# Performance work log

Measured on AMD Instinct MI355X. Metric: run time of the kernel, lower is better.

The kernel has to match this reference:

```python
import jax, jax.numpy as jnp
import numpy as np

D_MODEL = 1024
H = 16
D_K = D_MODEL // H
NEG_INF = -1e9


def setup_inputs() -> dict:
    key = jax.random.key(0)
    ks = jax.random.split(key, 12)
    B, S = 2, 2048
    s = 1.0 / np.sqrt(D_MODEL)
    inp = {
        "query": jax.random.normal(ks[0], (B, S, D_MODEL), jnp.float32),
        "key": jax.random.normal(ks[1], (B, S, D_MODEL), jnp.float32),
        "value": jax.random.normal(ks[2], (B, S, D_MODEL), jnp.float32),
        "mask": jnp.ones((B, 1, 1, S), jnp.int32),
        "w_q": jax.random.normal(ks[3], (D_MODEL, D_MODEL), jnp.float32) * s,
        "b_q": jax.random.normal(ks[4], (D_MODEL,), jnp.float32) * s,
        "w_k": jax.random.normal(ks[5], (D_MODEL, D_MODEL), jnp.float32) * s,
        "b_k": jax.random.normal(ks[6], (D_MODEL,), jnp.float32) * s,
        "w_v": jax.random.normal(ks[7], (D_MODEL, D_MODEL), jnp.float32) * s,
        "b_v": jax.random.normal(ks[8], (D_MODEL,), jnp.float32) * s,
        "w_o": jax.random.normal(ks[9], (D_MODEL, D_MODEL), jnp.float32) * s,
        "b_o": jax.random.normal(ks[10], (D_MODEL,), jnp.float32) * s,
    }
    return inp


def _split_heads(x):
    B, S, _ = x.shape
    return x.reshape(B, S, H, D_K).transpose(0, 2, 1, 3)  # (B,H,S,d_k)


def reference(query, key, value, mask, w_q, b_q, w_k, b_k, w_v, b_v, w_o, b_o):
    # torch Linear: y = x @ W^T + b
    q = _split_heads(query @ w_q.T + b_q)
    k = _split_heads(key @ w_k.T + b_k)
    v = _split_heads(value @ w_v.T + b_v)
    scale = 1.0 / jnp.sqrt(jnp.asarray(D_K, q.dtype))
    scores = jnp.einsum("bhqd,bhkd->bhqk", q, k) * scale  # (B,H,Sq,Sk)
    scores = jnp.where(mask == 0, jnp.asarray(NEG_INF, scores.dtype), scores)
    attn = jax.nn.softmax(scores, axis=-1)
    ctx = jnp.einsum("bhqk,bhkd->bhqd", attn, v)
    B, _, Sq, _ = ctx.shape
    ctx = ctx.transpose(0, 2, 1, 3).reshape(B, Sq, D_MODEL)
    out = ctx @ w_o.T + b_o
    return out, attn
```

## Files before the change

kernel.cpp:

```cpp
#include <hip/hip_runtime.h>
#include <math.h>

#define MDIM 4096
#define NDIM 1024
#define KDIM 1024
#define S_LEN 2048
#define NH 16
#define DK 64
#define KT 64
#define QT 64
#define NTILE (S_LEN / KT)

__global__ __launch_bounds__(256)
void gemm_nt_kernel(const float* __restrict__ A, const float* __restrict__ W,
                    const float* __restrict__ bias, float* __restrict__ Y,
                    int split_head)
{
    __shared__ float As[16][68];
    __shared__ float Ws[16][68];
    const int tid = threadIdx.x;
    const int m0 = blockIdx.y << 6;
    const int n0 = blockIdx.x << 6;
    const int tx = tid & 15;
    const int ty = tid >> 4;

    float acc[4][4] = {};

    for (int k0 = 0; k0 < KDIM; k0 += 16) {
        #pragma unroll
        for (int i = 0; i < 4; i++) {
            int e = tid + (i << 8);
            int r = e >> 4;
            int c = e & 15;
            As[c][r] = A[(m0 + r) * KDIM + k0 + c];
            Ws[c][r] = W[(n0 + r) * KDIM + k0 + c];
        }
        __syncthreads();
        #pragma unroll
        for (int kk = 0; kk < 16; kk++) {
            float a[4], w[4];
            #pragma unroll
            for (int i = 0; i < 4; i++) a[i] = As[kk][ty * 4 + i];
            #pragma unroll
            for (int j = 0; j < 4; j++) w[j] = Ws[kk][tx * 4 + j];
            #pragma unroll
            for (int i = 0; i < 4; i++)
                #pragma unroll
                for (int j = 0; j < 4; j++)
                    acc[i][j] += a[i] * w[j];
        }
        __syncthreads();
    }

    #pragma unroll
    for (int i = 0; i < 4; i++) {
        int m = m0 + ty * 4 + i;
        #pragma unroll
        for (int j = 0; j < 4; j++) {
            int n = n0 + tx * 4 + j;
            float val = acc[i][j] + bias[n];
            if (split_head) {
                int b = m >> 11, s = m & (S_LEN - 1);
                int h = n >> 6,  d = n & (DK - 1);
                Y[(((size_t)(b * NH + h) * S_LEN + s) << 6) + d] = val;
            } else {
                Y[(size_t)m * NDIM + n] = val;
            }
        }
    }
}

__global__ __launch_bounds__(256, 3)
void attn_kernel(const float* __restrict__ q, const float* __restrict__ k,
                 const float* __restrict__ v, const int* __restrict__ mask,
                 float* __restrict__ attn, float* __restrict__ ctx)
{
    const int b   = blockIdx.z;
    const int h   = blockIdx.y;
    const int q0  = blockIdx.x << 6;
    const int tid = threadIdx.x;
    const int tx  = tid & 15;
    const int ty  = tid >> 4;

    __shared__ float Qs[64][68];
    __shared__ float Ks[64][68];
    __shared__ float Vs[64][68];
    float* Ps = &Ks[0][0];

    const float* qbase = q + (((size_t)(b * NH + h) * S_LEN + q0) << 6);
    const float* kbase = k + (((size_t)(b * NH + h) * S_LEN) << 6);
    const float* vbase = v + (((size_t)(b * NH + h) * S_LEN) << 6);
    const int*   mrow  = mask + b * S_LEN;

    const int ln = tid & 63;
    const int dg = tid >> 6;

    {
        const float4* src = (const float4*)(qbase + ((size_t)ln << 6) + (dg << 4));
        #pragma unroll
        for (int c4 = 0; c4 < 4; c4++) {
            float4 t = src[c4];
            int d = (dg << 4) + (c4 << 2);
            Qs[d + 0][ln] = t.x; Qs[d + 1][ln] = t.y;
            Qs[d + 2][ln] = t.z; Qs[d + 3][ln] = t.w;
        }
    }

    const float scale = 0.125f;
    float mr[4], lr[4];
    #pragma unroll
    for (int i = 0; i < 4; i++) { mr[i] = -1e30f; lr[i] = 0.f; }

    for (int t = 0; t < NTILE; t++) {
        float4 kr[4];
        {
            const float4* src = (const float4*)(kbase + (((size_t)(t << 6) + ln) << 6) + (dg << 4));
            #pragma unroll
            for (int c4 = 0; c4 < 4; c4++) kr[c4] = src[c4];
        }
        __syncthreads();
        #pragma unroll
        for (int c4 = 0; c4 < 4; c4++) {
            int d = (dg << 4) + (c4 << 2);
            Ks[d + 0][ln] = kr[c4].x; Ks[d + 1][ln] = kr[c4].y;
            Ks[d + 2][ln] = kr[c4].z; Ks[d + 3][ln] = kr[c4].w;
        }
        __syncthreads();

        float s[4][4] = {};
        #pragma unroll 8
        for (int kk = 0; kk < 64; kk++) {
            float a[4], w[4];
            *(float4*)a = *(const float4*)&Qs[kk][ty << 2];
            *(float4*)w = *(const float4*)&Ks[kk][tx << 2];
            #pragma unroll
            for (int i = 0; i < 4; i++)
                #pragma unroll
                for (int j = 0; j < 4; j++)
                    s[i][j] += a[i] * w[j];
        }

        int4 mk = ((const int4*)(mrow + (t << 6)))[tx];
        #pragma unroll
        for (int i = 0; i < 4; i++) {
            float s0 = (mk.x == 0) ? -1e9f : s[i][0] * scale;
            float s1 = (mk.y == 0) ? -1e9f : s[i][1] * scale;
            float s2 = (mk.z == 0) ? -1e9f : s[i][2] * scale;
            float s3 = (mk.w == 0) ? -1e9f : s[i][3] * scale;
            float mt = fmaxf(fmaxf(s0, s1), fmaxf(s2, s3));
            float mn = fmaxf(mr[i], mt);
            lr[i] = lr[i] * __expf(mr[i] - mn)
                  + __expf(s0 - mn) + __expf(s1 - mn)
                  + __expf(s2 - mn) + __expf(s3 - mn);
            mr[i] = mn;
        }
    }

    #pragma unroll
    for (int off = 1; off < 16; off <<= 1) {
        #pragma unroll
        for (int i = 0; i < 4; i++) {
            float m2 = __shfl_xor(mr[i], off);
            float l2 = __shfl_xor(lr[i], off);
            float mn = fmaxf(mr[i], m2);
            lr[i] = lr[i] * __expf(mr[i] - mn) + l2 * __expf(m2 - mn);
            mr[i] = mn;
        }
    }
    float invl[4];
    #pragma unroll
    for (int i = 0; i < 4; i++) invl[i] = 1.0f / lr[i];

    float acc[4][4] = {};
    for (int t = 0; t < NTILE; t++) {
        float4 kr[4], vr[4];
        {
            const float4* src = (const float4*)(kbase + (((size_t)(t << 6) + ln) << 6) + (dg << 4));
            #pragma unroll
            for (int c4 = 0; c4 < 4; c4++) kr[c4] = src[c4];
        }
        #pragma unroll
        for (int i2 = 0; i2 < 4; i2++) {
            int slot = tid + (i2 << 8);
            int row = slot >> 4, c4 = slot & 15;
            vr[i2] = ((const float4*)(vbase + (((size_t)(t << 6) + row) << 6)))[c4];
        }
        __syncthreads();
        #pragma unroll
        for (int c4 = 0; c4 < 4; c4++) {
            int d = (dg << 4) + (c4 << 2);
            Ks[d + 0][ln] = kr[c4].x; Ks[d + 1][ln] = kr[c4].y;
            Ks[d + 2][ln] = kr[c4].z; Ks[d + 3][ln] = kr[c4].w;
        }
        #pragma unroll
        for (int i2 = 0; i2 < 4; i2++) {
            int slot = tid + (i2 << 8);
            int row = slot >> 4, c4 = slot & 15;
            *(float4*)&Vs[row][c4 << 2] = vr[i2];
        }
        __syncthreads();

        float s[4][4] = {};
        #pragma unroll 8
        for (int kk = 0; kk < 64; kk++) {
            float a[4], w[4];
            *(float4*)a = *(const float4*)&Qs[kk][ty << 2];
            *(float4*)w = *(const float4*)&Ks[kk][tx << 2];
            #pragma unroll
            for (int i = 0; i < 4; i++)
                #pragma unroll
                for (int j = 0; j < 4; j++)
                    s[i][j] += a[i] * w[j];
        }

        int4 mk = ((const int4*)(mrow + (t << 6)))[tx];
        float p[4][4];
        #pragma unroll
        for (int i = 0; i < 4; i++) {
            float s0 = (mk.x == 0) ? -1e9f : s[i][0] * scale;
            float s1 = (mk.y == 0) ? -1e9f : s[i][1] * scale;
            float s2 = (mk.z == 0) ? -1e9f : s[i][2] * scale;
            float s3 = (mk.w == 0) ? -1e9f : s[i][3] * scale;
            p[i][0] = __expf(s0 - mr[i]) * invl[i];
            p[i][1] = __expf(s1 - mr[i]) * invl[i];
            p[i][2] = __expf(s2 - mr[i]) * invl[i];
            p[i][3] = __expf(s3 - mr[i]) * invl[i];
        }

        {
            size_t arow = ((size_t)((b * NH + h) * S_LEN + q0 + (ty << 2))) * S_LEN
                        + (t << 6) + (tx << 2);
            #pragma unroll
            for (int i = 0; i < 4; i++)
                *(float4*)(attn + arow + (size_t)i * S_LEN) =
                    make_float4(p[i][0], p[i][1], p[i][2], p[i][3]);
        }

        __syncthreads();
        #pragma unroll
        for (int j = 0; j < 4; j++)
            *(float4*)&Ps[(size_t)((tx << 2) + j) * 68 + (ty << 2)] =
                make_float4(p[0][j], p[1][j], p[2][j], p[3][j]);
        __syncthreads();

        #pragma unroll 8
        for (int kk = 0; kk < 64; kk++) {
            float pa[4], wv[4];
            *(float4*)pa = *(const float4*)&Ps[(size_t)kk * 68 + (ty << 2)];
            *(float4*)wv = *(const float4*)&Vs[kk][tx << 2];
            #pragma unroll
            for (int i = 0; i < 4; i++)
                #pragma unroll
                for (int j = 0; j < 4; j++)
                    acc[i][j] += pa[i] * wv[j];
        }
    }

    #pragma unroll
    for (int i = 0; i < 4; i++) {
        int row = q0 + (ty << 2) + i;
        *(float4*)(ctx + (((size_t)(b * S_LEN + row) * NH + h) << 6) + (tx << 2)) =
            make_float4(acc[i][0], acc[i][1], acc[i][2], acc[i][3]);
    }
}

extern "C" void kernel_launch(void* const* d_in, const int* in_sizes, int n_in,
                              void* d_out, int out_size, void* d_ws, size_t ws_size,
                              hipStream_t stream)
{
    const float* query = (const float*)d_in[0];
    const float* key   = (const float*)d_in[1];
    const float* value = (const float*)d_in[2];
    const int*   mask  = (const int*)d_in[3];
    const float* w_q = (const float*)d_in[4];
    const float* b_q = (const float*)d_in[5];
    const float* w_k = (const float*)d_in[6];
    const float* b_k = (const float*)d_in[7];
    const float* w_v = (const float*)d_in[8];
    const float* b_v = (const float*)d_in[9];
    const float* w_o = (const float*)d_in[10];
    const float* b_o = (const float*)d_in[11];

    float* out  = (float*)d_out;
    float* attn = (float*)d_out + (size_t)4194304;

    float* qws  = (float*)d_ws;
    float* kws  = qws + 4194304;
    float* vws  = kws + 4194304;
    float* ctxw = vws + 4194304;

    dim3 gemm_grid(NDIM / 64, MDIM / 64);
    dim3 block(256);

    hipLaunchKernelGGL(gemm_nt_kernel, gemm_grid, block, 0, stream, query, w_q, b_q, qws, 1);
    hipLaunchKernelGGL(gemm_nt_kernel, gemm_grid, block, 0, stream, key,   w_k, b_k, kws, 1);
    hipLaunchKernelGGL(gemm_nt_kernel, gemm_grid, block, 0, stream, value, w_v, b_v, vws, 1);

    dim3 attn_grid(S_LEN / QT, NH, 2);
    hipLaunchKernelGGL(attn_kernel, attn_grid, block, 0, stream, qws, kws, vws, mask, attn, ctxw);

    hipLaunchKernelGGL(gemm_nt_kernel, gemm_grid, block, 0, stream, ctxw, w_o, b_o, out, 0);
}
```

Baseline: 1.783 ms.

## Cache masked scores in attn buffer to skip QK recompute; prefetch tiles in GEMM

The attention kernel now writes the scaled, masked scores into the attn output during the first (max/sum) pass. The second pass reads them back instead of reloading K and recomputing QK^T, then overwrites them with normalized probabilities. V reuses the Q shared buffer to free LDS, and occupancy hints are raised to 4. The projection GEMM now uses 64-wide K tiles with register prefetch of the next tile and float4 LDS reads. This trades the second QK matmul for an extra full write and read of the large attn matrix through global memory.

```diff
diff --git a/kernel.cpp b/kernel.cpp
--- a/kernel.cpp
+++ b/kernel.cpp
@@ -11,53 +11,65 @@
 #define QT 64
 #define NTILE (S_LEN / KT)
 
-__global__ __launch_bounds__(256)
+__global__ __launch_bounds__(256, 4)
 void gemm_nt_kernel(const float* __restrict__ A, const float* __restrict__ W,
                     const float* __restrict__ bias, float* __restrict__ Y,
                     int split_head)
 {
-    __shared__ float As[16][68];
-    __shared__ float Ws[16][68];
+    __shared__ float As[64][68];
+    __shared__ float Ws[64][68];
     const int tid = threadIdx.x;
     const int m0 = blockIdx.y << 6;
     const int n0 = blockIdx.x << 6;
     const int tx = tid & 15;
     const int ty = tid >> 4;
+    const int srow = tid >> 2;
+    const int sc4  = tid & 3;
+
+    const float4* asrc = (const float4*)(A + (size_t)(m0 + srow) * KDIM) + sc4;
+    const float4* wsrc = (const float4*)(W + (size_t)(n0 + srow) * KDIM) + sc4;
+
+    float4 ar[4], wr[4];
+    #pragma unroll
+    for (int i = 0; i < 4; i++) { ar[i] = asrc[i << 2]; wr[i] = wsrc[i << 2]; }
 
     float acc[4][4] = {};
 
-    for (int k0 = 0; k0 < KDIM; k0 += 16) {
-        #pragma unroll
-        for (int i = 0; i < 4; i++) {
-            int e = tid + (i << 8);
-            int r = e >> 4;
-            int c = e & 15;
-            As[c][r] = A[(m0 + r) * KDIM + k0 + c];
-            Ws[c][r] = W[(n0 + r) * KDIM + k0 + c];
-        }
-        __syncthreads();
-        #pragma unroll
-        for (int kk = 0; kk < 16; kk++) {
+    for (int k0 = 0; k0 < KDIM; k0 += 64) {
+        __syncthreads();
+        #pragma unroll
+        for (int i = 0; i < 4; i++) {
+            int d = (sc4 + (i << 2)) << 2;
+            As[d + 0][srow] = ar[i].x; As[d + 1][srow] = ar[i].y;
+            As[d + 2][srow] = ar[i].z; As[d + 3][srow] = ar[i].w;
+            Ws[d + 0][srow] = wr[i].x; Ws[d + 1][srow] = wr[i].y;
+            Ws[d + 2][srow] = wr[i].z; Ws[d + 3][srow] = wr[i].w;
+        }
+        __syncthreads();
+        if (k0 + 64 < KDIM) {
+            asrc += 16; wsrc += 16;
+            #pragma unroll
+            for (int i = 0; i < 4; i++) { ar[i] = asrc[i << 2]; wr[i] = wsrc[i << 2]; }
+        }
+        #pragma unroll 8
+        for (int kk = 0; kk < 64; kk++) {
             float a[4], w[4];
-            #pragma unroll
-            for (int i = 0; i < 4; i++) a[i] = As[kk][ty * 4 + i];
-            #pragma unroll
-            for (int j = 0; j < 4; j++) w[j] = Ws[kk][tx * 4 + j];
+            *(float4*)a = *(const float4*)&As[kk][ty << 2];
+            *(float4*)w = *(const float4*)&Ws[kk][tx << 2];
             #pragma unroll
             for (int i = 0; i < 4; i++)
                 #pragma unroll
                 for (int j = 0; j < 4; j++)
                     acc[i][j] += a[i] * w[j];
         }
-        __syncthreads();
     }
 
     #pragma unroll
     for (int i = 0; i < 4; i++) {
-        int m = m0 + ty * 4 + i;
+        int m = m0 + (ty << 2) + i;
         #pragma unroll
         for (int j = 0; j < 4; j++) {
-            int n = n0 + tx * 4 + j;
+            int n = n0 + (tx << 2) + j;
             float val = acc[i][j] + bias[n];
             if (split_head) {
                 int b = m >> 11, s = m & (S_LEN - 1);
@@ -70,7 +82,7 @@
     }
 }
 
-__global__ __launch_bounds__(256, 3)
+__global__ __launch_bounds__(256, 4)
 void attn_kernel(const float* __restrict__ q, const float* __restrict__ k,
                  const float* __restrict__ v, const int* __restrict__ mask,
                  float* __restrict__ attn, float* __restrict__ ctx)
@@ -84,7 +96,7 @@
 
     __shared__ float Qs[64][68];
     __shared__ float Ks[64][68];
-    __shared__ float Vs[64][68];
+    float (*Vs)[68] = Qs;
     float* Ps = &Ks[0][0];
 
     const float* qbase = q + (((size_t)(b * NH + h) * S_LEN + q0) << 6);
@@ -92,17 +104,17 @@
     const float* vbase = v + (((size_t)(b * NH + h) * S_LEN) << 6);
     const int*   mrow  = mask + b * S_LEN;
 
-    const int ln = tid & 63;
-    const int dg = tid >> 6;
+    const int srow = tid >> 2;
+    const int sc4  = tid & 3;
 
     {
-        const float4* src = (const float4*)(qbase + ((size_t)ln << 6) + (dg << 4));
-        #pragma unroll
-        for (int c4 = 0; c4 < 4; c4++) {
-            float4 t = src[c4];
-            int d = (dg << 4) + (c4 << 2);
-            Qs[d + 0][ln] = t.x; Qs[d + 1][ln] = t.y;
-            Qs[d + 2][ln] = t.z; Qs[d + 3][ln] = t.w;
+        const float4* src = (const float4*)(qbase + ((size_t)srow << 6)) + sc4;
+        #pragma unroll
+        for (int i = 0; i < 4; i++) {
+            float4 t = src[i << 2];
+            int d = (sc4 + (i << 2)) << 2;
+            Qs[d + 0][srow] = t.x; Qs[d + 1][srow] = t.y;
+            Qs[d + 2][srow] = t.z; Qs[d + 3][srow] = t.w;
         }
     }
 
@@ -111,21 +123,28 @@
     #pragma unroll
     for (int i = 0; i < 4; i++) { mr[i] = -1e30f; lr[i] = 0.f; }
 
+    const size_t abase = ((size_t)((b * NH + h) * S_LEN + q0 + (ty << 2))) * S_LEN
+                       + (tx << 2);
+
+    const float4* ksrc = (const float4*)(kbase + ((size_t)srow << 6)) + sc4;
+    float4 kr[4];
+    #pragma unroll
+    for (int i = 0; i < 4; i++) kr[i] = ksrc[i << 2];
+
     for (int t = 0; t < NTILE; t++) {
-        float4 kr[4];
-        {
-            const float4* src = (const float4*)(kbase + (((size_t)(t << 6) + ln) << 6) + (dg << 4));
-            #pragma unroll
-            for (int c4 = 0; c4 < 4; c4++) kr[c4] = src[c4];
-        }
-        __syncthreads();
-        #pragma unroll
-        for (int c4 = 0; c4 < 4; c4++) {
-            int d = (dg << 4) + (c4 << 2);
-            Ks[d + 0][ln] = kr[c4].x; Ks[d + 1][ln] = kr[c4].y;
-            Ks[d + 2][ln] = kr[c4].z; Ks[d + 3][ln] = kr[c4].w;
-        }
-        __syncthreads();
+        __syncthreads();
+        #pragma unroll
+        for (int i = 0; i < 4; i++) {
+            int d = (sc4 + (i << 2)) << 2;
+            Ks[d + 0][srow] = kr[i].x; Ks[d + 1][srow] = kr[i].y;
+            Ks[d + 2][srow] = kr[i].z; Ks[d + 3][srow] = kr[i].w;
+        }
+        __syncthreads();
+        if (t + 1 < NTILE) {
+            ksrc += 1024;
+            #pragma unroll
+            for (int i = 0; i < 4; i++) kr[i] = ksrc[i << 2];
+        }
 
         float s[4][4] = {};
         #pragma unroll 8
@@ -143,16 +162,18 @@
         int4 mk = ((const int4*)(mrow + (t << 6)))[tx];
         #pragma unroll
         for (int i = 0; i < 4; i++) {
-            float s0 = (mk.x == 0) ? -1e9f : s[i][0] * scale;
-            float s1 = (mk.y == 0) ? -1e9f : s[i][1] * scale;
-            float s2 = (mk.z == 0) ? -1e9f : s[i][2] * scale;
-            float s3 = (mk.w == 0) ? -1e9f : s[i][3] * scale;
-            float mt = fmaxf(fmaxf(s0, s1), fmaxf(s2, s3));
+            s[i][0] = (mk.x == 0) ? -1e9f : s[i][0] * scale;
+            s[i][1] = (mk.y == 0) ? -1e9f : s[i][1] * scale;
+            s[i][2] = (mk.z == 0) ? -1e9f : s[i][2] * scale;
+            s[i][3] = (mk.w == 0) ? -1e9f : s[i][3] * scale;
+            float mt = fmaxf(fmaxf(s[i][0], s[i][1]), fmaxf(s[i][2], s[i][3]));
             float mn = fmaxf(mr[i], mt);
             lr[i] = lr[i] * __expf(mr[i] - mn)
-                  + __expf(s0 - mn) + __expf(s1 - mn)
-                  + __expf(s2 - mn) + __expf(s3 - mn);
+                  + __expf(s[i][0] - mn) + __expf(s[i][1] - mn)
+                  + __expf(s[i][2] - mn) + __expf(s[i][3] - mn);
             mr[i] = mn;
+            *(float4*)(attn + abase + (t << 6) + (size_t)i * S_LEN) =
+                make_float4(s[i][0], s[i][1], s[i][2], s[i][3]);
         }
     }
 
@@ -171,77 +192,48 @@
     #pragma unroll
     for (int i = 0; i < 4; i++) invl[i] = 1.0f / lr[i];
 
+    const int vrow = tid >> 4;
+    const int vc4  = tid & 15;
+
     float acc[4][4] = {};
+    float4 vr[4], sr[4];
+    #pragma unroll
+    for (int i = 0; i < 4; i++) {
+        vr[i] = ((const float4*)(vbase + (((size_t)(vrow + (i << 4))) << 6)))[vc4];
+        sr[i] = *(const float4*)(attn + abase + (size_t)i * S_LEN);
+    }
+
     for (int t = 0; t < NTILE; t++) {
-        float4 kr[4], vr[4];
-        {
-            const float4* src = (const float4*)(kbase + (((size_t)(t << 6) + ln) << 6) + (dg << 4));
-            #pragma unroll
-            for (int c4 = 0; c4 < 4; c4++) kr[c4] = src[c4];
-        }
-        #pragma unroll
-        for (int i2 = 0; i2 < 4; i2++) {
-            int slot = tid + (i2 << 8);
-            int row = slot >> 4, c4 = slot & 15;
-            vr[i2] = ((const float4*)(vbase + (((size_t)(t << 6) + row) << 6)))[c4];
-        }
-        __syncthreads();
-        #pragma unroll
-        for (int c4 = 0; c4 < 4; c4++) {
-            int d = (dg << 4) + (c4 << 2);
-            Ks[d + 0][ln] = kr[c4].x; Ks[d + 1][ln] = kr[c4].y;
-            Ks[d + 2][ln] = kr[c4].z; Ks[d + 3][ln] = kr[c4].w;
-        }
-        #pragma unroll
-        for (int i2 = 0; i2 < 4; i2++) {
-            int slot = tid + (i2 << 8);
-            int row = slot >> 4, c4 = slot & 15;
-            *(float4*)&Vs[row][c4 << 2] = vr[i2];
-        }
-        __syncthreads();
-
-        float s[4][4] = {};
-        #pragma unroll 8
-        for (int kk = 0; kk < 64; kk++) {
-            float a[4], w[4];
-            *(float4*)a = *(const float4*)&Qs[kk][ty << 2];
-            *(float4*)w = *(const float4*)&Ks[kk][tx << 2];
-            #pragma unroll
-            for (int i = 0; i < 4; i++)
-                #pragma unroll
-                for (int j = 0; j < 4; j++)
-                    s[i][j] += a[i] * w[j];
-        }
-
-        int4 mk = ((const int4*)(mrow + (t << 6)))[tx];
+        __syncthreads();
+        #pragma unroll
+        for (int i = 0; i < 4; i++)
+            *(float4*)&Vs[vrow + (i << 4)][vc4 << 2] = vr[i];
+
         float p[4][4];
         #pragma unroll
         for (int i = 0; i < 4; i++) {
-            float s0 = (mk.x == 0) ? -1e9f : s[i][0] * scale;
-            float s1 = (mk.y == 0) ? -1e9f : s[i][1] * scale;
-            float s2 = (mk.z == 0) ? -1e9f : s[i][2] * scale;
-            float s3 = (mk.w == 0) ? -1e9f : s[i][3] * scale;
-            p[i][0] = __expf(s0 - mr[i]) * invl[i];
-            p[i][1] = __expf(s1 - mr[i]) * invl[i];
-            p[i][2] = __expf(s2 - mr[i]) * invl[i];
-            p[i][3] = __expf(s3 - mr[i]) * invl[i];
-        }
-
-        {
-            size_t arow = ((size_t)((b * NH + h) * S_LEN + q0 + (ty << 2))) * S_LEN
-                        + (t << 6) + (tx << 2);
-            #pragma unroll
-            for (int i = 0; i < 4; i++)
-                *(float4*)(attn + arow + (size_t)i * S_LEN) =
-                    make_float4(p[i][0], p[i][1], p[i][2], p[i][3]);
-        }
-
-        __syncthreads();
+            p[i][0] = __expf(sr[i].x - mr[i]) * invl[i];
+            p[i][1] = __expf(sr[i].y - mr[i]) * invl[i];
+            p[i][2] = __expf(sr[i].z - mr[i]) * invl[i];
+            p[i][3] = __expf(sr[i].w - mr[i]) * invl[i];
+            *(float4*)(attn + abase + (t << 6) + (size_t)i * S_LEN) =
+                make_float4(p[i][0], p[i][1], p[i][2], p[i][3]);
+        }
         #pragma unroll
         for (int j = 0; j < 4; j++)
             *(float4*)&Ps[(size_t)((tx << 2) + j) * 68 + (ty << 2)] =
                 make_float4(p[0][j], p[1][j], p[2][j], p[3][j]);
         __syncthreads();
+
+        if (t + 1 < NTILE) {
+            #pragma unroll
+            for (int i = 0; i < 4; i++) {
+                vr[i] = ((const float4*)(vbase +
+                          ((((size_t)(t + 1) << 6) + vrow + (i << 4)) << 6)))[vc4];
+                sr[i] = *(const float4*)(attn + abase + ((t + 1) << 6)
+                                         + (size_t)i * S_LEN);
+            }
+        }
 
         #pragma unroll 8
         for (int kk = 0; kk < 64; kk++) {
```

New measurement: 1.651 ms. 1.08x faster.
